# Kernel optimization log

Measured on AMD Instinct MI355X. Metric: run time of the kernel, lower is better.

## Reference

```python
import jax, jax.numpy as jnp
import numpy as np

N = 50000       # num nodes
E = 800000      # num edges
F_NODE = 128    # input node feature dim
F_EDGE = 32     # input edge feature dim
H = 64          # hidden dim (heads=1)
NEG_SLOPE = 0.2 # GAT leaky-relu slope


def _segment_softmax(scores, seg, num_segments):
    # numerically stable softmax over edges grouped by destination node
    m = jax.ops.segment_max(scores, seg, num_segments=num_segments)
    ex = jnp.exp(scores - m[seg])
    denom = jax.ops.segment_sum(ex, seg, num_segments=num_segments)
    return ex / (denom[seg] + 1e-16)


def _egat_conv(x, src, dst, eattr, W, We, a_src, a_dst, a_e, b):
    # PyG-style GAT layer with edge features (heads=1, no self loops).
    xp = x @ W                      # [N, H] projected nodes
    ep = eattr @ We                 # [E, H] projected edges (returned as new edge feats)
    score = (xp @ a_src)[src] + (xp @ a_dst)[dst] + ep @ a_e  # [E]
    score = jax.nn.leaky_relu(score, NEG_SLOPE)
    alpha = _segment_softmax(score, dst, N)                    # [E]
    out = jax.ops.segment_sum(alpha[:, None] * xp[src], dst, num_segments=N) + b
    return out, alpha, ep


def setup_inputs() -> dict:
    key = jax.random.key(0)
    ks = jax.random.split(key, 24)
    inp = {
        "x": jax.random.normal(ks[0], (N, F_NODE), jnp.float32),
        "edge_index": jax.random.randint(ks[1], (2, E), 0, N, jnp.int64),
        "edge_attr": jax.random.normal(ks[2], (E, F_EDGE), jnp.float32),
    }
    def glorot(k, shape):
        fan = shape[0] + shape[-1]
        return jax.random.normal(k, shape, jnp.float32) * jnp.sqrt(2.0 / fan)
    dims = [(F_NODE, F_EDGE), (H, H), (H, H)]
    i = 3
    for li, (din, dedge) in enumerate(dims, start=1):
        inp[f"W{li}"] = glorot(ks[i], (din, H)); i += 1
        inp[f"We{li}"] = glorot(ks[i], (dedge, H)); i += 1
        inp[f"as{li}"] = glorot(ks[i], (H,)); i += 1
        inp[f"ad{li}"] = glorot(ks[i], (H,)); i += 1
        inp[f"ae{li}"] = glorot(ks[i], (H,)); i += 1
        inp[f"b{li}"] = jnp.zeros((H,), jnp.float32)
    inp["Wc"] = glorot(ks[i], (H, 1)); i += 1
    inp["bc"] = jnp.zeros((1,), jnp.float32)
    return inp


def reference(x, edge_index, edge_attr,
              W1, We1, as1, ad1, ae1, b1,
              W2, We2, as2, ad2, ae2, b2,
              W3, We3, as3, ad3, ae3, b3,
              Wc, bc):
    src, dst = edge_index[0], edge_index[1]
    # layer 1 (edge feats projected F_EDGE -> H, reused as next edge_attr)
    x1, _, e1 = _egat_conv(x, src, dst, edge_attr, W1, We1, as1, ad1, ae1, b1)
    x1 = jax.nn.relu(x1)  # dropout is identity in eval mode
    # layer 2
    x2, _, e2 = _egat_conv(x1, src, dst, e1, W2, We2, as2, ad2, ae2, b2)
    x2 = jax.nn.relu(x2)
    # layer 3
    x3, _, _ = _egat_conv(x2, src, dst, e2, W3, We3, as3, ad3, ae3, b3)
    x3 = jax.nn.relu(x3)
    return x3 @ Wc + bc  # [N, 1]
```

## Files before the change

kernel.cpp:

```cpp
#include <hip/hip_runtime.h>
#include <hip/hip_fp16.h>
#include <math.h>

#define NN 50000
#define NE 800000
#define FN 128
#define FE 32
#define HD 64
#define NB 49
#define GP ((NN + 127) / 128)
#define EB ((NE + 511) / 512)

typedef unsigned long long u64;
typedef unsigned short u16;

__global__ void k_vecs_zero(const float* __restrict__ We1, const float* __restrict__ We2,
                            const float* __restrict__ We3, const float* __restrict__ ae1,
                            const float* __restrict__ ae2, const float* __restrict__ ae3,
                            float* __restrict__ v123, int* __restrict__ deg) {
  const int i = blockIdx.x * blockDim.x + threadIdx.x;
  if (i < NN) deg[i] = 0;
  if (blockIdx.x != 0) return;
  __shared__ float u2[HD], u3[HD], u23[HD];
  const int t = threadIdx.x;
  if (t < HD) {
    float s2 = 0.f, s3 = 0.f;
    for (int j = 0; j < HD; ++j) {
      s2 += We2[t * HD + j] * ae2[j];
      s3 += We3[t * HD + j] * ae3[j];
    }
    u2[t] = s2; u3[t] = s3;
  }
  __syncthreads();
  if (t < HD) {
    float s23 = 0.f;
    for (int j = 0; j < HD; ++j) s23 += We2[t * HD + j] * u3[j];
    u23[t] = s23;
  }
  __syncthreads();
  if (t < FE) {
    float a = 0.f, b = 0.f, c = 0.f;
    for (int j = 0; j < HD; ++j) {
      float w = We1[t * HD + j];
      a += w * ae1[j];
      b += w * u2[j];
      c += w * u23[j];
    }
    v123[t] = a; v123[32 + t] = b; v123[64 + t] = c;
  }
}

__device__ __forceinline__ u64 make_trec(const float* __restrict__ eattr,
                                         const float* __restrict__ v123,
                                         int s, int e) {
  const float4* ea = (const float4*)(eattr + (size_t)e * FE);
  float a = 0.f, b = 0.f, c = 0.f;
#pragma unroll
  for (int q = 0; q < FE / 4; ++q) {
    float4 xv = ea[q];
    const float* v1 = v123 + q * 4;
    const float* v2 = v123 + 32 + q * 4;
    const float* v3 = v123 + 64 + q * 4;
    a += xv.x * v1[0] + xv.y * v1[1] + xv.z * v1[2] + xv.w * v1[3];
    b += xv.x * v2[0] + xv.y * v2[1] + xv.z * v2[2] + xv.w * v2[3];
    c += xv.x * v3[0] + xv.y * v3[1] + xv.z * v3[2] + xv.w * v3[3];
  }
  return (u64)(u16)s
       | ((u64)__half_as_ushort(__float2half_rn(a)) << 16)
       | ((u64)__half_as_ushort(__float2half_rn(b)) << 32)
       | ((u64)__half_as_ushort(__float2half_rn(c)) << 48);
}

__global__ __launch_bounds__(256, 8) void k_edge(
    const int* __restrict__ srcA, const int* __restrict__ dstA,
    const float* __restrict__ eattr, const float* __restrict__ v123,
    int* __restrict__ deg, u16* __restrict__ rank, u64* __restrict__ trec) {
  const int t = threadIdx.x;
  const int base = blockIdx.x * 512;
  const int e0 = base + t;
  const int e1 = base + 256 + t;
  const bool ok0 = e0 < NE, ok1 = e1 < NE;

  int d0 = 0, d1 = 0, s0 = 0, s1 = 0;
  if (ok0) d0 = dstA[e0];
  if (ok1) d1 = dstA[e1];
  int r0 = 0, r1 = 0;
  if (ok0) r0 = atomicAdd(&deg[d0], 1);
  if (ok1) r1 = atomicAdd(&deg[d1], 1);
  if (ok0) s0 = srcA[e0];
  if (ok1) s1 = srcA[e1];

  if (ok0) trec[e0] = make_trec(eattr, v123, s0, e0);
  if (ok1) trec[e1] = make_trec(eattr, v123, s1, e1);

  if (ok0) rank[e0] = (u16)r0;
  if (ok1) rank[e1] = (u16)r1;
}

__global__ __launch_bounds__(256) void k_scanA(const int* __restrict__ deg,
                                               int* __restrict__ bsum) {
  __shared__ int ws[4];
  const int t = threadIdx.x, lane = t & 63, wid = t >> 6;
  const int i0 = blockIdx.x * 1024 + t * 4;
  int s = 0;
#pragma unroll
  for (int j = 0; j < 4; ++j) {
    int i = i0 + j;
    if (i < NN) s += deg[i];
  }
#pragma unroll
  for (int off = 32; off; off >>= 1) s += __shfl_xor(s, off);
  if (lane == 0) ws[wid] = s;
  __syncthreads();
  if (t == 0) bsum[blockIdx.x] = ws[0] + ws[1] + ws[2] + ws[3];
}

__global__ __launch_bounds__(256) void k_scanB(const int* __restrict__ deg,
                                               const int* __restrict__ bsum,
                                               int* __restrict__ row_ptr) {
  __shared__ int blockOff;
  __shared__ int wOff[4];
  const int b = blockIdx.x;
  const int t = threadIdx.x, lane = t & 63, wid = t >> 6;
  if (t < 64) {
    int v = (t < NB) ? bsum[t] : 0;
    int p = v;
#pragma unroll
    for (int off = 1; off < 64; off <<= 1) {
      int u = __shfl_up(p, off);
      if (lane >= off) p += u;
    }
    if (t == b) blockOff = p - v;
    if (b == 0 && t == NB - 1) row_ptr[NN] = p;
  }
  __syncthreads();
  const int i0 = b * 1024 + t * 4;
  int v[4];
#pragma unroll
  for (int j = 0; j < 4; ++j) {
    int i = i0 + j;
    v[j] = (i < NN) ? deg[i] : 0;
  }
  int s = v[0] + v[1] + v[2] + v[3];
  int p = s;
#pragma unroll
  for (int off = 1; off < 64; off <<= 1) {
    int u = __shfl_up(p, off);
    if (lane >= off) p += u;
  }
  if (lane == 63) wOff[wid] = p;
  __syncthreads();
  int woff = 0;
  for (int wq = 0; wq < wid; ++wq) woff += wOff[wq];
  int excl = blockOff + woff + (p - s);
#pragma unroll
  for (int j = 0; j < 4; ++j) {
    int i = i0 + j;
    if (i < NN) row_ptr[i] = excl;
    excl += v[j];
  }
}

__global__ __launch_bounds__(256) void k_gemm_scatter(
    const float* __restrict__ x, const float* __restrict__ W,
    const float* __restrict__ asv, const float* __restrict__ adv,
    __half* __restrict__ xph, float* __restrict__ ssrc, float* __restrict__ sdst,
    const int* __restrict__ dstA, const u16* __restrict__ rank,
    const int* __restrict__ row_ptr, const u64* __restrict__ trec,
    u64* __restrict__ aos) {
  const int t = threadIdx.x;
  if (blockIdx.x >= GP) {
    const int base = (blockIdx.x - GP) * 512;
    const int e0 = base + t;
    const int e1 = base + 256 + t;
    if (e0 < NE) aos[row_ptr[dstA[e0]] + (int)rank[e0]] = trec[e0];
    if (e1 < NE) aos[row_ptr[dstA[e1]] + (int)rank[e1]] = trec[e1];
    return;
  }
  const int w = t >> 6, l = t & 63;
  const int g = w * 4 + (l >> 4);
  const int rr = g * 8;
  const int c0 = (l & 15) * 4;
  const int row0 = blockIdx.x * 128;

  int xoff[8];
#pragma unroll
  for (int i = 0; i < 8; ++i) {
    int gr = row0 + rr + i;
    xoff[i] = (gr < NN ? gr : NN - 1) * FN;
  }

  float acc[8][4];
#pragma unroll
  for (int i = 0; i < 8; ++i)
#pragma unroll
    for (int j = 0; j < 4; ++j) acc[i][j] = 0.f;

  for (int k = 0; k < FN; k += 4) {
    float wv[4][4];
#pragma unroll
    for (int kk = 0; kk < 4; ++kk) {
      float4 wq = *(const float4*)(W + (k + kk) * HD + c0);
      wv[kk][0] = wq.x; wv[kk][1] = wq.y; wv[kk][2] = wq.z; wv[kk][3] = wq.w;
    }
#pragma unroll
    for (int i = 0; i < 8; ++i) {
      float4 a = *(const float4*)(x + xoff[i] + k);
#pragma unroll
      for (int j = 0; j < 4; ++j)
        acc[i][j] += a.x * wv[0][j] + a.y * wv[1][j] + a.z * wv[2][j] + a.w * wv[3][j];
    }
  }

  float as4[4], ad4[4];
#pragma unroll
  for (int j = 0; j < 4; ++j) { as4[j] = asv[c0 + j]; ad4[j] = adv[c0 + j]; }
#pragma unroll
  for (int i = 0; i < 8; ++i) {
    int gr = row0 + rr + i;
    float ps = 0.f, pd = 0.f;
#pragma unroll
    for (int j = 0; j < 4; ++j) {
      ps += acc[i][j] * as4[j];
      pd += acc[i][j] * ad4[j];
    }
#pragma unroll
    for (int off = 1; off < 16; off <<= 1) {
      ps += __shfl_xor(ps, off);
      pd += __shfl_xor(pd, off);
    }
    if (gr < NN) {
      union { __half2 h2[2]; float2 f2; } u;
      u.h2[0] = __floats2half2_rn(acc[i][0], acc[i][1]);
      u.h2[1] = __floats2half2_rn(acc[i][2], acc[i][3]);
      *(float2*)(xph + (size_t)gr * HD + c0) = u.f2;
      if ((l & 15) == 0) { ssrc[gr] = ps; sdst[gr] = pd; }
    }
  }
}

template <int TSEL>
__global__ __launch_bounds__(256) void k_agg_proj(
    const int* __restrict__ row_ptr, const u64* __restrict__ aos,
    const __half* __restrict__ xin, const float* __restrict__ ssrc_in,
    const float* __restrict__ sdst_in, const float* __restrict__ bias,
    const float* __restrict__ Wn, const float* __restrict__ asn,
    const float* __restrict__ adn, __half* __restrict__ xout,
    float* __restrict__ ssrc_out, float* __restrict__ sdst_out) {
  __shared__ __half swh[HD * HD];
  const int t = threadIdx.x;
  for (int i = t; i < HD * HD; i += 256) swh[i] = __float2half_rn(Wn[i]);

  const int gw = (blockIdx.x * blockDim.x + t) >> 6;
  const int lane = t & 63;
  const int g = lane >> 3;
  const int q = lane & 7;
  const int n = gw * 8 + g;
  const bool act = n < NN;
  int beg = 0, end = 0;
  float sd = 0.f;
  if (act) { beg = row_ptr[n]; end = row_ptr[n + 1]; sd = sdst_in[n]; }

  float dsum = 0.f;
  float4 o0 = make_float4(0.f, 0.f, 0.f, 0.f);
  float4 o1 = make_float4(0.f, 0.f, 0.f, 0.f);
  for (int base = beg; base < end; base += 16) {
    const int p0 = base + q, p1 = base + 8 + q;
    float pe0 = 0.f, pe1 = 0.f;
    int s0 = 0, s1 = 0;
    if (p0 < end) {
      u64 r = aos[p0];
      s0 = (int)(r & 0xFFFFu);
      float tt = __half2float(__ushort_as_half((u16)((r >> (16 * TSEL)) & 0xFFFFu)));
      float raw = ssrc_in[s0] + sd + tt;
      raw = raw > 0.f ? raw : 0.2f * raw;
      pe0 = __expf(raw);
    }
    if (p1 < end) {
      u64 r = aos[p1];
      s1 = (int)(r & 0xFFFFu);
      float tt = __half2float(__ushort_as_half((u16)((r >> (16 * TSEL)) & 0xFFFFu)));
      float raw = ssrc_in[s1] + sd + tt;
      raw = raw > 0.f ? raw : 0.2f * raw;
      pe1 = __expf(raw);
    }
    dsum += pe0 + pe1;
#pragma unroll
    for (int j = 0; j < 8; ++j) {
      const int sl = g * 8 + j;
      float pa = __shfl(pe0, sl);
      int sa = __shfl(s0, sl);
      float pb = __shfl(pe1, sl);
      int sb = __shfl(s1, sl);
      union { float4 f4; __half2 h2[4]; } ua, ub;
      ua.f4 = ((const float4*)(xin + (size_t)sa * HD))[q];
      ub.f4 = ((const float4*)(xin + (size_t)sb * HD))[q];
      float2 a0 = __half22float2(ua.h2[0]);
      float2 a1 = __half22float2(ua.h2[1]);
      float2 a2 = __half22float2(ua.h2[2]);
      float2 a3 = __half22float2(ua.h2[3]);
      o0.x += pa * a0.x; o0.y += pa * a0.y; o0.z += pa * a1.x; o0.w += pa * a1.y;
      o1.x += pa * a2.x; o1.y += pa * a2.y; o1.z += pa * a3.x; o1.w += pa * a3.y;
      float2 b0 = __half22float2(ub.h2[0]);
      float2 b1 = __half22float2(ub.h2[1]);
      float2 b2 = __half22float2(ub.h2[2]);
      float2 b3 = __half22float2(ub.h2[3]);
      o0.x += pb * b0.x; o0.y += pb * b0.y; o0.z += pb * b1.x; o0.w += pb * b1.y;
      o1.x += pb * b2.x; o1.y += pb * b2.y; o1.z += pb * b3.x; o1.w += pb * b3.y;
    }
  }
#pragma unroll
  for (int off = 1; off < 8; off <<= 1) dsum += __shfl_xor(dsum, off);

  const float inv = 1.f / (dsum + 1e-16f);
  const float4 b0 = ((const float4*)bias)[q * 2];
  const float4 b1 = ((const float4*)bias)[q * 2 + 1];
  float vreg[8];
  vreg[0] = fmaxf(o0.x * inv + b0.x, 0.f);
  vreg[1] = fmaxf(o0.y * inv + b0.y, 0.f);
  vreg[2] = fmaxf(o0.z * inv + b0.z, 0.f);
  vreg[3] = fmaxf(o0.w * inv + b0.w, 0.f);
  vreg[4] = fmaxf(o1.x * inv + b1.x, 0.f);
  vreg[5] = fmaxf(o1.y * inv + b1.y, 0.f);
  vreg[6] = fmaxf(o1.z * inv + b1.z, 0.f);
  vreg[7] = fmaxf(o1.w * inv + b1.w, 0.f);

  __syncthreads();

  float out8[8] = {0.f, 0.f, 0.f, 0.f, 0.f, 0.f, 0.f, 0.f};
#pragma unroll
  for (int kq = 0; kq < 8; ++kq) {
#pragma unroll
    for (int m = 0; m < 8; ++m) {
      float vb = __shfl(vreg[m], (lane & 56) | kq);
      union { float4 f4; __half2 h2[4]; } uw;
      uw.f4 = *(const float4*)(swh + (kq * 8 + m) * HD + q * 8);
      float2 w0 = __half22float2(uw.h2[0]);
      float2 w1 = __half22float2(uw.h2[1]);
      float2 w2 = __half22float2(uw.h2[2]);
      float2 w3 = __half22float2(uw.h2[3]);
      out8[0] += vb * w0.x; out8[1] += vb * w0.y;
      out8[2] += vb * w1.x; out8[3] += vb * w1.y;
      out8[4] += vb * w2.x; out8[5] += vb * w2.y;
      out8[6] += vb * w3.x; out8[7] += vb * w3.y;
    }
  }

  float ps = 0.f, pd = 0.f;
#pragma unroll
  for (int j = 0; j < 8; ++j) {
    ps += out8[j] * asn[q * 8 + j];
    pd += out8[j] * adn[q * 8 + j];
  }
#pragma unroll
  for (int off = 1; off < 8; off <<= 1) {
    ps += __shfl_xor(ps, off);
    pd += __shfl_xor(pd, off);
  }

  if (!act) return;
  union { float4 f4; __half2 h2[4]; } wv;
  wv.h2[0] = __floats2half2_rn(out8[0], out8[1]);
  wv.h2[1] = __floats2half2_rn(out8[2], out8[3]);
  wv.h2[2] = __floats2half2_rn(out8[4], out8[5]);
  wv.h2[3] = __floats2half2_rn(out8[6], out8[7]);
  ((float4*)(xout + (size_t)n * HD))[q] = wv.f4;
  if (q == 0) { ssrc_out[n] = ps; sdst_out[n] = pd; }
}

template <int TSEL>
__global__ __launch_bounds__(256) void k_agg_head(
    const int* __restrict__ row_ptr, const u64* __restrict__ aos,
    const __half* __restrict__ xin, const float* __restrict__ ssrc_in,
    const float* __restrict__ sdst_in, const float* __restrict__ bias,
    const float* __restrict__ Wc, const float* __restrict__ bc,
    float* __restrict__ outf) {
  const int gw = (blockIdx.x * blockDim.x + threadIdx.x) >> 6;
  const int lane = threadIdx.x & 63;
  const int g = lane >> 3;
  const int q = lane & 7;
  const int n = gw * 8 + g;
  const bool act = n < NN;
  int beg = 0, end = 0;
  float sd = 0.f;
  if (act) { beg = row_ptr[n]; end = row_ptr[n + 1]; sd = sdst_in[n]; }

  float dsum = 0.f;
  float4 o0 = make_float4(0.f, 0.f, 0.f, 0.f);
  float4 o1 = make_float4(0.f, 0.f, 0.f, 0.f);
  for (int base = beg; base < end; base += 16) {
    const int p0 = base + q, p1 = base + 8 + q;
    float pe0 = 0.f, pe1 = 0.f;
    int s0 = 0, s1 = 0;
    if (p0 < end) {
      u64 r = aos[p0];
      s0 = (int)(r & 0xFFFFu);
      float tt = __half2float(__ushort_as_half((u16)((r >> (16 * TSEL)) & 0xFFFFu)));
      float raw = ssrc_in[s0] + sd + tt;
      raw = raw > 0.f ? raw : 0.2f * raw;
      pe0 = __expf(raw);
    }
    if (p1 < end) {
      u64 r = aos[p1];
      s1 = (int)(r & 0xFFFFu);
      float tt = __half2float(__ushort_as_half((u16)((r >> (16 * TSEL)) & 0xFFFFu)));
      float raw = ssrc_in[s1] + sd + tt;
      raw = raw > 0.f ? raw : 0.2f * raw;
      pe1 = __expf(raw);
    }
    dsum += pe0 + pe1;
#pragma unroll
    for (int j = 0; j < 8; ++j) {
      const int sl = g * 8 + j;
      float pa = __shfl(pe0, sl);
      int sa = __shfl(s0, sl);
      float pb = __shfl(pe1, sl);
      int sb = __shfl(s1, sl);
      union { float4 f4; __half2 h2[4]; } ua, ub;
      ua.f4 = ((const float4*)(xin + (size_t)sa * HD))[q];
      ub.f4 = ((const float4*)(xin + (size_t)sb * HD))[q];
      float2 a0 = __half22float2(ua.h2[0]);
      float2 a1 = __half22float2(ua.h2[1]);
      float2 a2 = __half22float2(ua.h2[2]);
      float2 a3 = __half22float2(ua.h2[3]);
      o0.x += pa * a0.x; o0.y += pa * a0.y; o0.z += pa * a1.x; o0.w += pa * a1.y;
      o1.x += pa * a2.x; o1.y += pa * a2.y; o1.z += pa * a3.x; o1.w += pa * a3.y;
      float2 b0 = __half22float2(ub.h2[0]);
      float2 b1 = __half22float2(ub.h2[1]);
      float2 b2 = __half22float2(ub.h2[2]);
      float2 b3 = __half22float2(ub.h2[3]);
      o0.x += pb * b0.x; o0.y += pb * b0.y; o0.z += pb * b1.x; o0.w += pb * b1.y;
      o1.x += pb * b2.x; o1.y += pb * b2.y; o1.z += pb * b3.x; o1.w += pb * b3.y;
    }
  }
#pragma unroll
  for (int off = 1; off < 8; off <<= 1) dsum += __shfl_xor(dsum, off);

  if (!act) return;
  const float inv = 1.f / (dsum + 1e-16f);
  const float4 b0 = ((const float4*)bias)[q * 2];
  const float4 b1 = ((const float4*)bias)[q * 2 + 1];
  const float4 w0 = ((const float4*)Wc)[q * 2];
  const float4 w1 = ((const float4*)Wc)[q * 2 + 1];
  float c = fmaxf(o0.x * inv + b0.x, 0.f) * w0.x +
            fmaxf(o0.y * inv + b0.y, 0.f) * w0.y +
            fmaxf(o0.z * inv + b0.z, 0.f) * w0.z +
            fmaxf(o0.w * inv + b0.w, 0.f) * w0.w +
            fmaxf(o1.x * inv + b1.x, 0.f) * w1.x +
            fmaxf(o1.y * inv + b1.y, 0.f) * w1.y +
            fmaxf(o1.z * inv + b1.z, 0.f) * w1.z +
            fmaxf(o1.w * inv + b1.w, 0.f) * w1.w;
#pragma unroll
  for (int off = 1; off < 8; off <<= 1) c += __shfl_xor(c, off);
  if (q == 0) outf[n] = c + bc[0];
}

extern "C" void kernel_launch(void* const* d_in, const int* in_sizes, int n_in,
                              void* d_out, int out_size, void* d_ws, size_t ws_size,
                              hipStream_t stream) {
  const float* x     = (const float*)d_in[0];
  const int*   ei    = (const int*)d_in[1];
  const float* eattr = (const float*)d_in[2];
  const float* W1  = (const float*)d_in[3];
  const float* We1 = (const float*)d_in[4];
  const float* as1 = (const float*)d_in[5];
  const float* ad1 = (const float*)d_in[6];
  const float* ae1 = (const float*)d_in[7];
  const float* b1  = (const float*)d_in[8];
  const float* W2  = (const float*)d_in[9];
  const float* We2 = (const float*)d_in[10];
  const float* as2 = (const float*)d_in[11];
  const float* ad2 = (const float*)d_in[12];
  const float* ae2 = (const float*)d_in[13];
  const float* b2  = (const float*)d_in[14];
  const float* W3  = (const float*)d_in[15];
  const float* We3 = (const float*)d_in[16];
  const float* as3 = (const float*)d_in[17];
  const float* ad3 = (const float*)d_in[18];
  const float* ae3 = (const float*)d_in[19];
  const float* b3  = (const float*)d_in[20];
  const float* Wc  = (const float*)d_in[21];
  const float* bc  = (const float*)d_in[22];

  const int* srcA = ei;
  const int* dstA = ei + NE;
  float* outf = (float*)d_out;

  char* w = (char*)d_ws;
  auto alloc = [&](size_t bytes) {
    char* p = w;
    w += (bytes + 255) & ~(size_t)255;
    return p;
  };
  float* v123 = (float*)alloc(96 * 4);
  u64* aos = (u64*)alloc((size_t)NE * 8);
  u64* trec = (u64*)alloc((size_t)NE * 8);
  u16* rank = (u16*)alloc((size_t)NE * 2);
  int* row_ptr = (int*)alloc((size_t)(NN + 1) * 4);
  int* deg = (int*)alloc((size_t)NN * 4);
  int* bsum = (int*)alloc((size_t)NB * 4);
  __half* xpA = (__half*)alloc((size_t)NN * HD * 2);
  __half* xpB = (__half*)alloc((size_t)NN * HD * 2);
  float* ssrcA = (float*)alloc((size_t)NN * 4);
  float* sdstA = (float*)alloc((size_t)NN * 4);
  float* ssrcB = (float*)alloc((size_t)NN * 4);
  float* sdstB = (float*)alloc((size_t)NN * 4);

  const int gN = (NN + 255) / 256;
  const int gA = ((NN + 7) / 8 * 64 + 255) / 256;

  k_vecs_zero<<<gN, 256, 0, stream>>>(We1, We2, We3, ae1, ae2, ae3, v123, deg);
  k_edge<<<EB, 256, 0, stream>>>(srcA, dstA, eattr, v123, deg, rank, trec);
  k_scanA<<<NB, 256, 0, stream>>>(deg, bsum);
  k_scanB<<<NB, 256, 0, stream>>>(deg, bsum, row_ptr);
  k_gemm_scatter<<<GP + EB, 256, 0, stream>>>(x, W1, as1, ad1, xpA, ssrcA, sdstA,
                                              dstA, rank, row_ptr, trec, aos);
  k_agg_proj<1><<<gA, 256, 0, stream>>>(row_ptr, aos, xpA, ssrcA, sdstA, b1,
                                        W2, as2, ad2, xpB, ssrcB, sdstB);
  k_agg_proj<2><<<gA, 256, 0, stream>>>(row_ptr, aos, xpB, ssrcB, sdstB, b2,
                                        W3, as3, ad3, xpA, ssrcA, sdstA);
  k_agg_head<3><<<gA, 256, 0, stream>>>(row_ptr, aos, xpA, ssrcA, sdstA, b3,
                                        Wc, bc, outf);
}
```

Baseline: 176.1 us.

## Privatize degree counters into sixteen slices and fuse layer-1 GEMM with edge pass

Degree counting now uses sixteen private copies of the counter array, one per group of edge blocks, so atomic contention on hot destination nodes is spread out. The scan kernels sum the slices and turn each slice into a per-slice base offset used by a new standalone scatter kernel. The layer-1 node GEMM moves from the scatter kernel into the edge/atomic kernel, so it runs in the same launch as the edge pass. In exchange the zeroing and scans touch sixteen times more counter memory, and the scan writes per-slice offsets with strided accesses.

```diff
diff --git a/kernel.cpp b/kernel.cpp
--- a/kernel.cpp
+++ b/kernel.cpp
@@ -7,6 +7,7 @@
 #define FN 128
 #define FE 32
 #define HD 64
+#define NS 16
 #define NB 49
 #define GP ((NN + 127) / 128)
 #define EB ((NE + 511) / 512)
@@ -19,7 +20,7 @@
                             const float* __restrict__ ae2, const float* __restrict__ ae3,
                             float* __restrict__ v123, int* __restrict__ deg) {
   const int i = blockIdx.x * blockDim.x + threadIdx.x;
-  if (i < NN) deg[i] = 0;
+  if (i < NS * NN) deg[i] = 0;
   if (blockIdx.x != 0) return;
   __shared__ float u2[HD], u3[HD], u23[HD];
   const int t = threadIdx.x;
@@ -71,30 +72,98 @@
        | ((u64)__half_as_ushort(__float2half_rn(c)) << 48);
 }
 
-__global__ __launch_bounds__(256, 8) void k_edge(
+__global__ __launch_bounds__(256) void k_mega2(
+    const float* __restrict__ x, const float* __restrict__ W,
+    const float* __restrict__ asv, const float* __restrict__ adv,
+    __half* __restrict__ xph, float* __restrict__ ssrc, float* __restrict__ sdst,
     const int* __restrict__ srcA, const int* __restrict__ dstA,
     const float* __restrict__ eattr, const float* __restrict__ v123,
     int* __restrict__ deg, u16* __restrict__ rank, u64* __restrict__ trec) {
   const int t = threadIdx.x;
-  const int base = blockIdx.x * 512;
-  const int e0 = base + t;
-  const int e1 = base + 256 + t;
-  const bool ok0 = e0 < NE, ok1 = e1 < NE;
-
-  int d0 = 0, d1 = 0, s0 = 0, s1 = 0;
-  if (ok0) d0 = dstA[e0];
-  if (ok1) d1 = dstA[e1];
-  int r0 = 0, r1 = 0;
-  if (ok0) r0 = atomicAdd(&deg[d0], 1);
-  if (ok1) r1 = atomicAdd(&deg[d1], 1);
-  if (ok0) s0 = srcA[e0];
-  if (ok1) s1 = srcA[e1];
-
-  if (ok0) trec[e0] = make_trec(eattr, v123, s0, e0);
-  if (ok1) trec[e1] = make_trec(eattr, v123, s1, e1);
-
-  if (ok0) rank[e0] = (u16)r0;
-  if (ok1) rank[e1] = (u16)r1;
+  if (blockIdx.x >= GP) {
+    const int k = blockIdx.x - GP;
+    const int base = k * 512;
+    const int psh = (k & (NS - 1)) * NN;
+    const int e0 = base + t;
+    const int e1 = base + 256 + t;
+    const bool ok0 = e0 < NE, ok1 = e1 < NE;
+
+    int d0 = 0, d1 = 0, s0 = 0, s1 = 0;
+    if (ok0) d0 = dstA[e0];
+    if (ok1) d1 = dstA[e1];
+    int r0 = 0, r1 = 0;
+    if (ok0) r0 = atomicAdd(&deg[psh + d0], 1);
+    if (ok1) r1 = atomicAdd(&deg[psh + d1], 1);
+    if (ok0) s0 = srcA[e0];
+    if (ok1) s1 = srcA[e1];
+
+    if (ok0) trec[e0] = make_trec(eattr, v123, s0, e0);
+    if (ok1) trec[e1] = make_trec(eattr, v123, s1, e1);
+
+    if (ok0) rank[e0] = (u16)r0;
+    if (ok1) rank[e1] = (u16)r1;
+    return;
+  }
+  const int w = t >> 6, l = t & 63;
+  const int g = w * 4 + (l >> 4);
+  const int rr = g * 8;
+  const int c0 = (l & 15) * 4;
+  const int row0 = blockIdx.x * 128;
+
+  int xoff[8];
+#pragma unroll
+  for (int i = 0; i < 8; ++i) {
+    int gr = row0 + rr + i;
+    xoff[i] = (gr < NN ? gr : NN - 1) * FN;
+  }
+
+  float acc[8][4];
+#pragma unroll
+  for (int i = 0; i < 8; ++i)
+#pragma unroll
+    for (int j = 0; j < 4; ++j) acc[i][j] = 0.f;
+
+  for (int k = 0; k < FN; k += 4) {
+    float wv[4][4];
+#pragma unroll
+    for (int kk = 0; kk < 4; ++kk) {
+      float4 wq = *(const float4*)(W + (k + kk) * HD + c0);
+      wv[kk][0] = wq.x; wv[kk][1] = wq.y; wv[kk][2] = wq.z; wv[kk][3] = wq.w;
+    }
+#pragma unroll
+    for (int i = 0; i < 8; ++i) {
+      float4 a = *(const float4*)(x + xoff[i] + k);
+#pragma unroll
+      for (int j = 0; j < 4; ++j)
+        acc[i][j] += a.x * wv[0][j] + a.y * wv[1][j] + a.z * wv[2][j] + a.w * wv[3][j];
+    }
+  }
+
+  float as4[4], ad4[4];
+#pragma unroll
+  for (int j = 0; j < 4; ++j) { as4[j] = asv[c0 + j]; ad4[j] = adv[c0 + j]; }
+#pragma unroll
+  for (int i = 0; i < 8; ++i) {
+    int gr = row0 + rr + i;
+    float ps = 0.f, pd = 0.f;
+#pragma unroll
+    for (int j = 0; j < 4; ++j) {
+      ps += acc[i][j] * as4[j];
+      pd += acc[i][j] * ad4[j];
+    }
+#pragma unroll
+    for (int off = 1; off < 16; off <<= 1) {
+      ps += __shfl_xor(ps, off);
+      pd += __shfl_xor(pd, off);
+    }
+    if (gr < NN) {
+      union { __half2 h2[2]; float2 f2; } u;
+      u.h2[0] = __floats2half2_rn(acc[i][0], acc[i][1]);
+      u.h2[1] = __floats2half2_rn(acc[i][2], acc[i][3]);
+      *(float2*)(xph + (size_t)gr * HD + c0) = u.f2;
+      if ((l & 15) == 0) { ssrc[gr] = ps; sdst[gr] = pd; }
+    }
+  }
 }
 
 __global__ __launch_bounds__(256) void k_scanA(const int* __restrict__ deg,
@@ -103,10 +172,12 @@
   const int t = threadIdx.x, lane = t & 63, wid = t >> 6;
   const int i0 = blockIdx.x * 1024 + t * 4;
   int s = 0;
-#pragma unroll
-  for (int j = 0; j < 4; ++j) {
-    int i = i0 + j;
-    if (i < NN) s += deg[i];
+  if (i0 < NN) {
+#pragma unroll
+    for (int p = 0; p < NS; ++p) {
+      int4 v = *(const int4*)(deg + p * NN + i0);
+      s += v.x + v.y + v.z + v.w;
+    }
   }
 #pragma unroll
   for (int off = 32; off; off >>= 1) s += __shfl_xor(s, off);
@@ -115,7 +186,7 @@
   if (t == 0) bsum[blockIdx.x] = ws[0] + ws[1] + ws[2] + ws[3];
 }
 
-__global__ __launch_bounds__(256) void k_scanB(const int* __restrict__ deg,
+__global__ __launch_bounds__(256) void k_scanB(int* __restrict__ deg,
                                                const int* __restrict__ bsum,
                                                int* __restrict__ row_ptr) {
   __shared__ int blockOff;
@@ -136,10 +207,16 @@
   __syncthreads();
   const int i0 = b * 1024 + t * 4;
   int v[4];
-#pragma unroll
-  for (int j = 0; j < 4; ++j) {
-    int i = i0 + j;
-    v[j] = (i < NN) ? deg[i] : 0;
+  if (i0 < NN) {
+    int4 acc = make_int4(0, 0, 0, 0);
+#pragma unroll
+    for (int p = 0; p < NS; ++p) {
+      int4 dv = *(const int4*)(deg + p * NN + i0);
+      acc.x += dv.x; acc.y += dv.y; acc.z += dv.z; acc.w += dv.w;
+    }
+    v[0] = acc.x; v[1] = acc.y; v[2] = acc.z; v[3] = acc.w;
+  } else {
+    v[0] = v[1] = v[2] = v[3] = 0;
   }
   int s = v[0] + v[1] + v[2] + v[3];
   int p = s;
@@ -156,87 +233,31 @@
 #pragma unroll
   for (int j = 0; j < 4; ++j) {
     int i = i0 + j;
-    if (i < NN) row_ptr[i] = excl;
-    excl += v[j];
-  }
-}
-
-__global__ __launch_bounds__(256) void k_gemm_scatter(
-    const float* __restrict__ x, const float* __restrict__ W,
-    const float* __restrict__ asv, const float* __restrict__ adv,
-    __half* __restrict__ xph, float* __restrict__ ssrc, float* __restrict__ sdst,
-    const int* __restrict__ dstA, const u16* __restrict__ rank,
-    const int* __restrict__ row_ptr, const u64* __restrict__ trec,
-    u64* __restrict__ aos) {
+    if (i < NN) {
+      row_ptr[i] = excl;
+      int run = excl;
+#pragma unroll
+      for (int ps = 0; ps < NS; ++ps) {
+        int dv = deg[ps * NN + i];
+        deg[ps * NN + i] = run;
+        run += dv;
+      }
+      excl += v[j];
+    }
+  }
+}
+
+__global__ void k_scatter(const int* __restrict__ dstA, const u16* __restrict__ rank,
+                          const int* __restrict__ sbase, const u64* __restrict__ trec,
+                          u64* __restrict__ aos) {
+  const int k = blockIdx.x;
+  const int base = k * 512;
+  const int psh = (k & (NS - 1)) * NN;
   const int t = threadIdx.x;
-  if (blockIdx.x >= GP) {
-    const int base = (blockIdx.x - GP) * 512;
-    const int e0 = base + t;
-    const int e1 = base + 256 + t;
-    if (e0 < NE) aos[row_ptr[dstA[e0]] + (int)rank[e0]] = trec[e0];
-    if (e1 < NE) aos[row_ptr[dstA[e1]] + (int)rank[e1]] = trec[e1];
-    return;
-  }
-  const int w = t >> 6, l = t & 63;
-  const int g = w * 4 + (l >> 4);
-  const int rr = g * 8;
-  const int c0 = (l & 15) * 4;
-  const int row0 = blockIdx.x * 128;
-
-  int xoff[8];
-#pragma unroll
-  for (int i = 0; i < 8; ++i) {
-    int gr = row0 + rr + i;
-    xoff[i] = (gr < NN ? gr : NN - 1) * FN;
-  }
-
-  float acc[8][4];
-#pragma unroll
-  for (int i = 0; i < 8; ++i)
-#pragma unroll
-    for (int j = 0; j < 4; ++j) acc[i][j] = 0.f;
-
-  for (int k = 0; k < FN; k += 4) {
-    float wv[4][4];
-#pragma unroll
-    for (int kk = 0; kk < 4; ++kk) {
-      float4 wq = *(const float4*)(W + (k + kk) * HD + c0);
-      wv[kk][0] = wq.x; wv[kk][1] = wq.y; wv[kk][2] = wq.z; wv[kk][3] = wq.w;
-    }
-#pragma unroll
-    for (int i = 0; i < 8; ++i) {
-      float4 a = *(const float4*)(x + xoff[i] + k);
-#pragma unroll
-      for (int j = 0; j < 4; ++j)
-        acc[i][j] += a.x * wv[0][j] + a.y * wv[1][j] + a.z * wv[2][j] + a.w * wv[3][j];
-    }
-  }
-
-  float as4[4], ad4[4];
-#pragma unroll
-  for (int j = 0; j < 4; ++j) { as4[j] = asv[c0 + j]; ad4[j] = adv[c0 + j]; }
-#pragma unroll
-  for (int i = 0; i < 8; ++i) {
-    int gr = row0 + rr + i;
-    float ps = 0.f, pd = 0.f;
-#pragma unroll
-    for (int j = 0; j < 4; ++j) {
-      ps += acc[i][j] * as4[j];
-      pd += acc[i][j] * ad4[j];
-    }
-#pragma unroll
-    for (int off = 1; off < 16; off <<= 1) {
-      ps += __shfl_xor(ps, off);
-      pd += __shfl_xor(pd, off);
-    }
-    if (gr < NN) {
-      union { __half2 h2[2]; float2 f2; } u;
-      u.h2[0] = __floats2half2_rn(acc[i][0], acc[i][1]);
-      u.h2[1] = __floats2half2_rn(acc[i][2], acc[i][3]);
-      *(float2*)(xph + (size_t)gr * HD + c0) = u.f2;
-      if ((l & 15) == 0) { ssrc[gr] = ps; sdst[gr] = pd; }
-    }
-  }
+  const int e0 = base + t;
+  const int e1 = base + 256 + t;
+  if (e0 < NE) aos[sbase[psh + dstA[e0]] + (int)rank[e0]] = trec[e0];
+  if (e1 < NE) aos[sbase[psh + dstA[e1]] + (int)rank[e1]] = trec[e1];
 }
 
 template <int TSEL>
@@ -497,7 +518,7 @@
   u64* trec = (u64*)alloc((size_t)NE * 8);
   u16* rank = (u16*)alloc((size_t)NE * 2);
   int* row_ptr = (int*)alloc((size_t)(NN + 1) * 4);
-  int* deg = (int*)alloc((size_t)NN * 4);
+  int* deg = (int*)alloc((size_t)NS * NN * 4);
   int* bsum = (int*)alloc((size_t)NB * 4);
   __half* xpA = (__half*)alloc((size_t)NN * HD * 2);
   __half* xpB = (__half*)alloc((size_t)NN * HD * 2);
@@ -506,15 +527,15 @@
   float* ssrcB = (float*)alloc((size_t)NN * 4);
   float* sdstB = (float*)alloc((size_t)NN * 4);
 
-  const int gN = (NN + 255) / 256;
+  const int gZ = (NS * NN + 255) / 256;
   const int gA = ((NN + 7) / 8 * 64 + 255) / 256;
 
-  k_vecs_zero<<<gN, 256, 0, stream>>>(We1, We2, We3, ae1, ae2, ae3, v123, deg);
-  k_edge<<<EB, 256, 0, stream>>>(srcA, dstA, eattr, v123, deg, rank, trec);
+  k_vecs_zero<<<gZ, 256, 0, stream>>>(We1, We2, We3, ae1, ae2, ae3, v123, deg);
+  k_mega2<<<GP + EB, 256, 0, stream>>>(x, W1, as1, ad1, xpA, ssrcA, sdstA,
+                                       srcA, dstA, eattr, v123, deg, rank, trec);
   k_scanA<<<NB, 256, 0, stream>>>(deg, bsum);
   k_scanB<<<NB, 256, 0, stream>>>(deg, bsum, row_ptr);
-  k_gemm_scatter<<<GP + EB, 256, 0, stream>>>(x, W1, as1, ad1, xpA, ssrcA, sdstA,
-                                              dstA, rank, row_ptr, trec, aos);
+  k_scatter<<<EB, 256, 0, stream>>>(dstA, rank, deg, trec, aos);
   k_agg_proj<1><<<gA, 256, 0, stream>>>(row_ptr, aos, xpA, ssrcA, sdstA, b1,
                                         W2, as2, ad2, xpB, ssrcB, sdstB);
   k_agg_proj<2><<<gA, 256, 0, stream>>>(row_ptr, aos, xpB, ssrcB, sdstB, b2,
```

Result: faster. 172.3 us (-2.1%).

## Replace global-atomic CSR build with two-pass bucketed radix partition by destination

Applied to the files above, without the earlier changes.

The CSR construction no longer does per-edge global atomics on a degree array. It now builds per-block shared-memory histograms over 196 coarse destination buckets of 256 nodes each, scans them, and scatters edge records into the buckets with shared atomics. A final per-bucket kernel does a local counting sort into the CSR array and writes row_ptr. This is meant to cut contended global atomics and the random scatter. In exchange it adds an extra pass over an intermediate 8-byte record buffer and produces a different within-row edge order.

```diff
diff --git a/kernel.cpp b/kernel.cpp
--- a/kernel.cpp
+++ b/kernel.cpp
@@ -7,48 +7,17 @@
 #define FN 128
 #define FE 32
 #define HD 64
-#define NB 49
+#define NBKT 196
+#define EPB 2048
+#define NSB ((NE + EPB - 1) / EPB)
+#define EPT (EPB / 256)
+#define CNT_N (NBKT * NSB)
+#define SCB 2048
+#define NB2 ((CNT_N + SCB - 1) / SCB)
 #define GP ((NN + 127) / 128)
-#define EB ((NE + 511) / 512)
 
 typedef unsigned long long u64;
 typedef unsigned short u16;
-
-__global__ void k_vecs_zero(const float* __restrict__ We1, const float* __restrict__ We2,
-                            const float* __restrict__ We3, const float* __restrict__ ae1,
-                            const float* __restrict__ ae2, const float* __restrict__ ae3,
-                            float* __restrict__ v123, int* __restrict__ deg) {
-  const int i = blockIdx.x * blockDim.x + threadIdx.x;
-  if (i < NN) deg[i] = 0;
-  if (blockIdx.x != 0) return;
-  __shared__ float u2[HD], u3[HD], u23[HD];
-  const int t = threadIdx.x;
-  if (t < HD) {
-    float s2 = 0.f, s3 = 0.f;
-    for (int j = 0; j < HD; ++j) {
-      s2 += We2[t * HD + j] * ae2[j];
-      s3 += We3[t * HD + j] * ae3[j];
-    }
-    u2[t] = s2; u3[t] = s3;
-  }
-  __syncthreads();
-  if (t < HD) {
-    float s23 = 0.f;
-    for (int j = 0; j < HD; ++j) s23 += We2[t * HD + j] * u3[j];
-    u23[t] = s23;
-  }
-  __syncthreads();
-  if (t < FE) {
-    float a = 0.f, b = 0.f, c = 0.f;
-    for (int j = 0; j < HD; ++j) {
-      float w = We1[t * HD + j];
-      a += w * ae1[j];
-      b += w * u2[j];
-      c += w * u23[j];
-    }
-    v123[t] = a; v123[32 + t] = b; v123[64 + t] = c;
-  }
-}
 
 __device__ __forceinline__ u64 make_trec(const float* __restrict__ eattr,
                                          const float* __restrict__ v123,
@@ -71,42 +40,65 @@
        | ((u64)__half_as_ushort(__float2half_rn(c)) << 48);
 }
 
-__global__ __launch_bounds__(256, 8) void k_edge(
-    const int* __restrict__ srcA, const int* __restrict__ dstA,
-    const float* __restrict__ eattr, const float* __restrict__ v123,
-    int* __restrict__ deg, u16* __restrict__ rank, u64* __restrict__ trec) {
+__global__ __launch_bounds__(256) void k_count(
+    const int* __restrict__ dstA, int* __restrict__ cnt,
+    const float* __restrict__ We1, const float* __restrict__ We2,
+    const float* __restrict__ We3, const float* __restrict__ ae1,
+    const float* __restrict__ ae2, const float* __restrict__ ae3,
+    float* __restrict__ v123) {
+  __shared__ int hist[NBKT];
   const int t = threadIdx.x;
-  const int base = blockIdx.x * 512;
-  const int e0 = base + t;
-  const int e1 = base + 256 + t;
-  const bool ok0 = e0 < NE, ok1 = e1 < NE;
-
-  int d0 = 0, d1 = 0, s0 = 0, s1 = 0;
-  if (ok0) d0 = dstA[e0];
-  if (ok1) d1 = dstA[e1];
-  int r0 = 0, r1 = 0;
-  if (ok0) r0 = atomicAdd(&deg[d0], 1);
-  if (ok1) r1 = atomicAdd(&deg[d1], 1);
-  if (ok0) s0 = srcA[e0];
-  if (ok1) s1 = srcA[e1];
-
-  if (ok0) trec[e0] = make_trec(eattr, v123, s0, e0);
-  if (ok1) trec[e1] = make_trec(eattr, v123, s1, e1);
-
-  if (ok0) rank[e0] = (u16)r0;
-  if (ok1) rank[e1] = (u16)r1;
-}
-
-__global__ __launch_bounds__(256) void k_scanA(const int* __restrict__ deg,
-                                               int* __restrict__ bsum) {
+  const int blk = blockIdx.x;
+  if (t < NBKT) hist[t] = 0;
+  __syncthreads();
+  const int base = blk * EPB;
+#pragma unroll 1
+  for (int it = 0; it < EPT; ++it) {
+    int e = base + it * 256 + t;
+    if (e < NE) atomicAdd(&hist[dstA[e] >> 8], 1);
+  }
+  __syncthreads();
+  if (t < NBKT) cnt[t * NSB + blk] = hist[t];
+
+  if (blk != 0) return;
+  __shared__ float u2[HD], u3[HD], u23[HD];
+  if (t < HD) {
+    float s2 = 0.f, s3 = 0.f;
+    for (int j = 0; j < HD; ++j) {
+      s2 += We2[t * HD + j] * ae2[j];
+      s3 += We3[t * HD + j] * ae3[j];
+    }
+    u2[t] = s2; u3[t] = s3;
+  }
+  __syncthreads();
+  if (t < HD) {
+    float s23 = 0.f;
+    for (int j = 0; j < HD; ++j) s23 += We2[t * HD + j] * u3[j];
+    u23[t] = s23;
+  }
+  __syncthreads();
+  if (t < FE) {
+    float a = 0.f, b = 0.f, c = 0.f;
+    for (int j = 0; j < HD; ++j) {
+      float w = We1[t * HD + j];
+      a += w * ae1[j];
+      b += w * u2[j];
+      c += w * u23[j];
+    }
+    v123[t] = a; v123[32 + t] = b; v123[64 + t] = c;
+  }
+}
+
+__global__ __launch_bounds__(256) void k_scanA2(const int* __restrict__ cnt,
+                                                int* __restrict__ bsum) {
   __shared__ int ws[4];
   const int t = threadIdx.x, lane = t & 63, wid = t >> 6;
-  const int i0 = blockIdx.x * 1024 + t * 4;
+  const int i0 = blockIdx.x * SCB + t * 8;
   int s = 0;
 #pragma unroll
-  for (int j = 0; j < 4; ++j) {
+  for (int j = 0; j < 8; ++j) {
     int i = i0 + j;
-    if (i < NN) s += deg[i];
+    if (i < CNT_N) s += cnt[i];
   }
 #pragma unroll
   for (int off = 32; off; off >>= 1) s += __shfl_xor(s, off);
@@ -115,15 +107,14 @@
   if (t == 0) bsum[blockIdx.x] = ws[0] + ws[1] + ws[2] + ws[3];
 }
 
-__global__ __launch_bounds__(256) void k_scanB(const int* __restrict__ deg,
-                                               const int* __restrict__ bsum,
-                                               int* __restrict__ row_ptr) {
+__global__ __launch_bounds__(256) void k_scanB2(int* __restrict__ cnt,
+                                                const int* __restrict__ bsum) {
   __shared__ int blockOff;
   __shared__ int wOff[4];
   const int b = blockIdx.x;
   const int t = threadIdx.x, lane = t & 63, wid = t >> 6;
   if (t < 64) {
-    int v = (t < NB) ? bsum[t] : 0;
+    int v = (t < NB2) ? bsum[t] : 0;
     int p = v;
 #pragma unroll
     for (int off = 1; off < 64; off <<= 1) {
@@ -131,17 +122,18 @@
       if (lane >= off) p += u;
     }
     if (t == b) blockOff = p - v;
-    if (b == 0 && t == NB - 1) row_ptr[NN] = p;
-  }
-  __syncthreads();
-  const int i0 = b * 1024 + t * 4;
-  int v[4];
-#pragma unroll
-  for (int j = 0; j < 4; ++j) {
+  }
+  __syncthreads();
+  const int i0 = b * SCB + t * 8;
+  int v[8];
+#pragma unroll
+  for (int j = 0; j < 8; ++j) {
     int i = i0 + j;
-    v[j] = (i < NN) ? deg[i] : 0;
-  }
-  int s = v[0] + v[1] + v[2] + v[3];
+    v[j] = (i < CNT_N) ? cnt[i] : 0;
+  }
+  int s = 0;
+#pragma unroll
+  for (int j = 0; j < 8; ++j) s += v[j];
   int p = s;
 #pragma unroll
   for (int off = 1; off < 64; off <<= 1) {
@@ -154,34 +146,47 @@
   for (int wq = 0; wq < wid; ++wq) woff += wOff[wq];
   int excl = blockOff + woff + (p - s);
 #pragma unroll
-  for (int j = 0; j < 4; ++j) {
+  for (int j = 0; j < 8; ++j) {
     int i = i0 + j;
-    if (i < NN) row_ptr[i] = excl;
-    excl += v[j];
-  }
-}
-
-__global__ __launch_bounds__(256) void k_gemm_scatter(
+    if (i < CNT_N) { cnt[i] = excl; excl += v[j]; }
+  }
+}
+
+__global__ __launch_bounds__(256) void k_mega3(
     const float* __restrict__ x, const float* __restrict__ W,
     const float* __restrict__ asv, const float* __restrict__ adv,
     __half* __restrict__ xph, float* __restrict__ ssrc, float* __restrict__ sdst,
-    const int* __restrict__ dstA, const u16* __restrict__ rank,
-    const int* __restrict__ row_ptr, const u64* __restrict__ trec,
-    u64* __restrict__ aos) {
+    const int* __restrict__ srcA, const int* __restrict__ dstA,
+    const float* __restrict__ eattr, const float* __restrict__ v123,
+    const int* __restrict__ gbase, u64* __restrict__ btrec,
+    u16* __restrict__ bdst) {
+  __shared__ int off[NBKT];
   const int t = threadIdx.x;
-  if (blockIdx.x >= GP) {
-    const int base = (blockIdx.x - GP) * 512;
-    const int e0 = base + t;
-    const int e1 = base + 256 + t;
-    if (e0 < NE) aos[row_ptr[dstA[e0]] + (int)rank[e0]] = trec[e0];
-    if (e1 < NE) aos[row_ptr[dstA[e1]] + (int)rank[e1]] = trec[e1];
+  if (blockIdx.x < NSB) {
+    const int blk = blockIdx.x;
+    if (t < NBKT) off[t] = gbase[t * NSB + blk];
+    __syncthreads();
+    const int base = blk * EPB;
+#pragma unroll 1
+    for (int it = 0; it < EPT; ++it) {
+      int e = base + it * 256 + t;
+      if (e < NE) {
+        int d = dstA[e];
+        int s = srcA[e];
+        u64 r = make_trec(eattr, v123, s, e);
+        int pos = atomicAdd(&off[d >> 8], 1);
+        btrec[pos] = r;
+        bdst[pos] = (u16)(d & 255);
+      }
+    }
     return;
   }
+  const int pb = blockIdx.x - NSB;
   const int w = t >> 6, l = t & 63;
   const int g = w * 4 + (l >> 4);
   const int rr = g * 8;
   const int c0 = (l & 15) * 4;
-  const int row0 = blockIdx.x * 128;
+  const int row0 = pb * 128;
 
   int xoff[8];
 #pragma unroll
@@ -225,9 +230,9 @@
       pd += acc[i][j] * ad4[j];
     }
 #pragma unroll
-    for (int off = 1; off < 16; off <<= 1) {
-      ps += __shfl_xor(ps, off);
-      pd += __shfl_xor(pd, off);
+    for (int off2 = 1; off2 < 16; off2 <<= 1) {
+      ps += __shfl_xor(ps, off2);
+      pd += __shfl_xor(pd, off2);
     }
     if (gr < NN) {
       union { __half2 h2[2]; float2 f2; } u;
@@ -236,6 +241,45 @@
       *(float2*)(xph + (size_t)gr * HD + c0) = u.f2;
       if ((l & 15) == 0) { ssrc[gr] = ps; sdst[gr] = pd; }
     }
+  }
+}
+
+__global__ __launch_bounds__(256) void k_bucket(
+    const int* __restrict__ gbase, const u64* __restrict__ btrec,
+    const u16* __restrict__ bdst, int* __restrict__ row_ptr,
+    u64* __restrict__ aos) {
+  __shared__ int hist[256], off2[256];
+  __shared__ int wsum[4];
+  const int b = blockIdx.x;
+  const int t = threadIdx.x, lane = t & 63, wid = t >> 6;
+  const int s = gbase[b * NSB];
+  const int e = (b + 1 < NBKT) ? gbase[(b + 1) * NSB] : NE;
+  hist[t] = 0;
+  __syncthreads();
+  for (int p = s + t; p < e; p += 256) atomicAdd(&hist[(int)bdst[p]], 1);
+  __syncthreads();
+  int v = hist[t];
+  int pfx = v;
+#pragma unroll
+  for (int o = 1; o < 64; o <<= 1) {
+    int u = __shfl_up(pfx, o);
+    if (lane >= o) pfx += u;
+  }
+  if (lane == 63) wsum[wid] = pfx;
+  __syncthreads();
+  int woff = 0;
+  for (int wq = 0; wq < wid; ++wq) woff += wsum[wq];
+  const int excl = woff + pfx - v;
+  off2[t] = excl;
+  const int n = b * 256 + t;
+  if (n < NN) row_ptr[n] = s + excl;
+  if (b == 0 && t == 0) row_ptr[NN] = NE;
+  __syncthreads();
+  for (int p = s + t; p < e; p += 256) {
+    u64 r = btrec[p];
+    int d8 = (int)bdst[p];
+    int pos = s + atomicAdd(&off2[d8], 1);
+    aos[pos] = r;
   }
 }
 
@@ -494,11 +538,11 @@
   };
   float* v123 = (float*)alloc(96 * 4);
   u64* aos = (u64*)alloc((size_t)NE * 8);
-  u64* trec = (u64*)alloc((size_t)NE * 8);
-  u16* rank = (u16*)alloc((size_t)NE * 2);
+  u64* btrec = (u64*)alloc((size_t)NE * 8);
+  u16* bdst = (u16*)alloc((size_t)NE * 2);
   int* row_ptr = (int*)alloc((size_t)(NN + 1) * 4);
-  int* deg = (int*)alloc((size_t)NN * 4);
-  int* bsum = (int*)alloc((size_t)NB * 4);
+  int* cnt = (int*)alloc((size_t)CNT_N * 4);
+  int* bsum = (int*)alloc((size_t)NB2 * 4);
   __half* xpA = (__half*)alloc((size_t)NN * HD * 2);
   __half* xpB = (__half*)alloc((size_t)NN * HD * 2);
   float* ssrcA = (float*)alloc((size_t)NN * 4);
@@ -506,15 +550,14 @@
   float* ssrcB = (float*)alloc((size_t)NN * 4);
   float* sdstB = (float*)alloc((size_t)NN * 4);
 
-  const int gN = (NN + 255) / 256;
   const int gA = ((NN + 7) / 8 * 64 + 255) / 256;
 
-  k_vecs_zero<<<gN, 256, 0, stream>>>(We1, We2, We3, ae1, ae2, ae3, v123, deg);
-  k_edge<<<EB, 256, 0, stream>>>(srcA, dstA, eattr, v123, deg, rank, trec);
-  k_scanA<<<NB, 256, 0, stream>>>(deg, bsum);
-  k_scanB<<<NB, 256, 0, stream>>>(deg, bsum, row_ptr);
-  k_gemm_scatter<<<GP + EB, 256, 0, stream>>>(x, W1, as1, ad1, xpA, ssrcA, sdstA,
-                                              dstA, rank, row_ptr, trec, aos);
+  k_count<<<NSB, 256, 0, stream>>>(dstA, cnt, We1, We2, We3, ae1, ae2, ae3, v123);
+  k_scanA2<<<NB2, 256, 0, stream>>>(cnt, bsum);
+  k_scanB2<<<NB2, 256, 0, stream>>>(cnt, bsum);
+  k_mega3<<<NSB + GP, 256, 0, stream>>>(x, W1, as1, ad1, xpA, ssrcA, sdstA,
+                                        srcA, dstA, eattr, v123, cnt, btrec, bdst);
+  k_bucket<<<NBKT, 256, 0, stream>>>(cnt, btrec, bdst, row_ptr, aos);
   k_agg_proj<1><<<gA, 256, 0, stream>>>(row_ptr, aos, xpA, ssrcA, sdstA, b1,
                                         W2, as2, ad2, xpB, ssrcB, sdstB);
   k_agg_proj<2><<<gA, 256, 0, stream>>>(row_ptr, aos, xpB, ssrcB, sdstB, b2,
```

New measurement: 171.3 us. 2.8% less time.

## Fuse layer-1 GEMM with edge pass; coalesce edge-attr loads via cooperative reduction

Applied to the files above, without the earlier changes.

Moves the layer-1 node projection GEMM into the same launch as the per-edge degree counting and score-term computation, and makes the CSR scatter its own kernel after the scan. The edge pass now has 8 lanes read one edge's 32 attributes cooperatively in contiguous float4 chunks and reduces with shuffles, replacing strided per-thread row reads. This is meant to overlap the compute-bound GEMM with the memory- and atomic-bound edge work and to coalesce edge_attr reads. In exchange it adds shuffle work, and the scatter stays a separate launch. NT=NE/64 assumes NE is divisible by 64, which holds here.

```diff
diff --git a/kernel.cpp b/kernel.cpp
--- a/kernel.cpp
+++ b/kernel.cpp
@@ -9,7 +9,9 @@
 #define HD 64
 #define NB 49
 #define GP ((NN + 127) / 128)
-#define EB ((NE + 511) / 512)
+#define NT (NE / 64)
+#define EB2 ((NT + 7) / 8)
+#define GE ((NE + 255) / 256)
 
 typedef unsigned long long u64;
 typedef unsigned short u16;
@@ -50,51 +52,116 @@
   }
 }
 
-__device__ __forceinline__ u64 make_trec(const float* __restrict__ eattr,
-                                         const float* __restrict__ v123,
-                                         int s, int e) {
-  const float4* ea = (const float4*)(eattr + (size_t)e * FE);
-  float a = 0.f, b = 0.f, c = 0.f;
-#pragma unroll
-  for (int q = 0; q < FE / 4; ++q) {
-    float4 xv = ea[q];
-    const float* v1 = v123 + q * 4;
-    const float* v2 = v123 + 32 + q * 4;
-    const float* v3 = v123 + 64 + q * 4;
-    a += xv.x * v1[0] + xv.y * v1[1] + xv.z * v1[2] + xv.w * v1[3];
-    b += xv.x * v2[0] + xv.y * v2[1] + xv.z * v2[2] + xv.w * v2[3];
-    c += xv.x * v3[0] + xv.y * v3[1] + xv.z * v3[2] + xv.w * v3[3];
-  }
-  return (u64)(u16)s
-       | ((u64)__half_as_ushort(__float2half_rn(a)) << 16)
-       | ((u64)__half_as_ushort(__float2half_rn(b)) << 32)
-       | ((u64)__half_as_ushort(__float2half_rn(c)) << 48);
-}
-
-__global__ __launch_bounds__(256, 8) void k_edge(
+__global__ __launch_bounds__(256) void k_mega4(
+    const float* __restrict__ x, const float* __restrict__ W,
+    const float* __restrict__ asv, const float* __restrict__ adv,
+    __half* __restrict__ xph, float* __restrict__ ssrc, float* __restrict__ sdst,
     const int* __restrict__ srcA, const int* __restrict__ dstA,
     const float* __restrict__ eattr, const float* __restrict__ v123,
     int* __restrict__ deg, u16* __restrict__ rank, u64* __restrict__ trec) {
   const int t = threadIdx.x;
-  const int base = blockIdx.x * 512;
-  const int e0 = base + t;
-  const int e1 = base + 256 + t;
-  const bool ok0 = e0 < NE, ok1 = e1 < NE;
-
-  int d0 = 0, d1 = 0, s0 = 0, s1 = 0;
-  if (ok0) d0 = dstA[e0];
-  if (ok1) d1 = dstA[e1];
-  int r0 = 0, r1 = 0;
-  if (ok0) r0 = atomicAdd(&deg[d0], 1);
-  if (ok1) r1 = atomicAdd(&deg[d1], 1);
-  if (ok0) s0 = srcA[e0];
-  if (ok1) s1 = srcA[e1];
-
-  if (ok0) trec[e0] = make_trec(eattr, v123, s0, e0);
-  if (ok1) trec[e1] = make_trec(eattr, v123, s1, e1);
-
-  if (ok0) rank[e0] = (u16)r0;
-  if (ok1) rank[e1] = (u16)r1;
+  if (blockIdx.x >= GP) {
+    const int kb = blockIdx.x - GP;
+    const int w = t >> 6, lane = t & 63;
+    const int g = lane >> 3, q = lane & 7;
+    const float4 v1q = *(const float4*)(v123 + q * 4);
+    const float4 v2q = *(const float4*)(v123 + 32 + q * 4);
+    const float4 v3q = *(const float4*)(v123 + 64 + q * 4);
+    const int perm = 8 * q + g;
+#pragma unroll
+    for (int it = 0; it < 2; ++it) {
+      const int tIdx = kb * 8 + w * 2 + it;
+      if (tIdx < NT) {
+        const int E0 = tIdx * 64;
+        const int e = E0 + perm;
+        const int d = dstA[e];
+        const int s = srcA[e];
+        const int r = atomicAdd(&deg[d], 1);
+        float ra = 0.f, rb = 0.f, rc = 0.f;
+#pragma unroll
+        for (int k = 0; k < 8; ++k) {
+          const float4 xv =
+              *(const float4*)(eattr + (size_t)(E0 + 8 * k + g) * FE + q * 4);
+          float a = xv.x * v1q.x + xv.y * v1q.y + xv.z * v1q.z + xv.w * v1q.w;
+          float b = xv.x * v2q.x + xv.y * v2q.y + xv.z * v2q.z + xv.w * v2q.w;
+          float c = xv.x * v3q.x + xv.y * v3q.y + xv.z * v3q.z + xv.w * v3q.w;
+#pragma unroll
+          for (int off = 1; off < 8; off <<= 1) {
+            a += __shfl_xor(a, off);
+            b += __shfl_xor(b, off);
+            c += __shfl_xor(c, off);
+          }
+          if (q == k) { ra = a; rb = b; rc = c; }
+        }
+        trec[e] = (u64)(u16)s
+                | ((u64)__half_as_ushort(__float2half_rn(ra)) << 16)
+                | ((u64)__half_as_ushort(__float2half_rn(rb)) << 32)
+                | ((u64)__half_as_ushort(__float2half_rn(rc)) << 48);
+        rank[e] = (u16)r;
+      }
+    }
+    return;
+  }
+  const int w = t >> 6, l = t & 63;
+  const int g = w * 4 + (l >> 4);
+  const int rr = g * 8;
+  const int c0 = (l & 15) * 4;
+  const int row0 = blockIdx.x * 128;
+
+  int xoff[8];
+#pragma unroll
+  for (int i = 0; i < 8; ++i) {
+    int gr = row0 + rr + i;
+    xoff[i] = (gr < NN ? gr : NN - 1) * FN;
+  }
+
+  float acc[8][4];
+#pragma unroll
+  for (int i = 0; i < 8; ++i)
+#pragma unroll
+    for (int j = 0; j < 4; ++j) acc[i][j] = 0.f;
+
+  for (int k = 0; k < FN; k += 4) {
+    float wv[4][4];
+#pragma unroll
+    for (int kk = 0; kk < 4; ++kk) {
+      float4 wq = *(const float4*)(W + (k + kk) * HD + c0);
+      wv[kk][0] = wq.x; wv[kk][1] = wq.y; wv[kk][2] = wq.z; wv[kk][3] = wq.w;
+    }
+#pragma unroll
+    for (int i = 0; i < 8; ++i) {
+      float4 a = *(const float4*)(x + xoff[i] + k);
+#pragma unroll
+      for (int j = 0; j < 4; ++j)
+        acc[i][j] += a.x * wv[0][j] + a.y * wv[1][j] + a.z * wv[2][j] + a.w * wv[3][j];
+    }
+  }
+
+  float as4[4], ad4[4];
+#pragma unroll
+  for (int j = 0; j < 4; ++j) { as4[j] = asv[c0 + j]; ad4[j] = adv[c0 + j]; }
+#pragma unroll
+  for (int i = 0; i < 8; ++i) {
+    int gr = row0 + rr + i;
+    float ps = 0.f, pd = 0.f;
+#pragma unroll
+    for (int j = 0; j < 4; ++j) {
+      ps += acc[i][j] * as4[j];
+      pd += acc[i][j] * ad4[j];
+    }
+#pragma unroll
+    for (int off = 1; off < 16; off <<= 1) {
+      ps += __shfl_xor(ps, off);
+      pd += __shfl_xor(pd, off);
+    }
+    if (gr < NN) {
+      union { __half2 h2[2]; float2 f2; } u;
+      u.h2[0] = __floats2half2_rn(acc[i][0], acc[i][1]);
+      u.h2[1] = __floats2half2_rn(acc[i][2], acc[i][3]);
+      *(float2*)(xph + (size_t)gr * HD + c0) = u.f2;
+      if ((l & 15) == 0) { ssrc[gr] = ps; sdst[gr] = pd; }
+    }
+  }
 }
 
 __global__ __launch_bounds__(256) void k_scanA(const int* __restrict__ deg,
@@ -161,82 +228,12 @@
   }
 }
 
-__global__ __launch_bounds__(256) void k_gemm_scatter(
-    const float* __restrict__ x, const float* __restrict__ W,
-    const float* __restrict__ asv, const float* __restrict__ adv,
-    __half* __restrict__ xph, float* __restrict__ ssrc, float* __restrict__ sdst,
-    const int* __restrict__ dstA, const u16* __restrict__ rank,
-    const int* __restrict__ row_ptr, const u64* __restrict__ trec,
-    u64* __restrict__ aos) {
-  const int t = threadIdx.x;
-  if (blockIdx.x >= GP) {
-    const int base = (blockIdx.x - GP) * 512;
-    const int e0 = base + t;
-    const int e1 = base + 256 + t;
-    if (e0 < NE) aos[row_ptr[dstA[e0]] + (int)rank[e0]] = trec[e0];
-    if (e1 < NE) aos[row_ptr[dstA[e1]] + (int)rank[e1]] = trec[e1];
-    return;
-  }
-  const int w = t >> 6, l = t & 63;
-  const int g = w * 4 + (l >> 4);
-  const int rr = g * 8;
-  const int c0 = (l & 15) * 4;
-  const int row0 = blockIdx.x * 128;
-
-  int xoff[8];
-#pragma unroll
-  for (int i = 0; i < 8; ++i) {
-    int gr = row0 + rr + i;
-    xoff[i] = (gr < NN ? gr : NN - 1) * FN;
-  }
-
-  float acc[8][4];
-#pragma unroll
-  for (int i = 0; i < 8; ++i)
-#pragma unroll
-    for (int j = 0; j < 4; ++j) acc[i][j] = 0.f;
-
-  for (int k = 0; k < FN; k += 4) {
-    float wv[4][4];
-#pragma unroll
-    for (int kk = 0; kk < 4; ++kk) {
-      float4 wq = *(const float4*)(W + (k + kk) * HD + c0);
-      wv[kk][0] = wq.x; wv[kk][1] = wq.y; wv[kk][2] = wq.z; wv[kk][3] = wq.w;
-    }
-#pragma unroll
-    for (int i = 0; i < 8; ++i) {
-      float4 a = *(const float4*)(x + xoff[i] + k);
-#pragma unroll
-      for (int j = 0; j < 4; ++j)
-        acc[i][j] += a.x * wv[0][j] + a.y * wv[1][j] + a.z * wv[2][j] + a.w * wv[3][j];
-    }
-  }
-
-  float as4[4], ad4[4];
-#pragma unroll
-  for (int j = 0; j < 4; ++j) { as4[j] = asv[c0 + j]; ad4[j] = adv[c0 + j]; }
-#pragma unroll
-  for (int i = 0; i < 8; ++i) {
-    int gr = row0 + rr + i;
-    float ps = 0.f, pd = 0.f;
-#pragma unroll
-    for (int j = 0; j < 4; ++j) {
-      ps += acc[i][j] * as4[j];
-      pd += acc[i][j] * ad4[j];
-    }
-#pragma unroll
-    for (int off = 1; off < 16; off <<= 1) {
-      ps += __shfl_xor(ps, off);
-      pd += __shfl_xor(pd, off);
-    }
-    if (gr < NN) {
-      union { __half2 h2[2]; float2 f2; } u;
-      u.h2[0] = __floats2half2_rn(acc[i][0], acc[i][1]);
-      u.h2[1] = __floats2half2_rn(acc[i][2], acc[i][3]);
-      *(float2*)(xph + (size_t)gr * HD + c0) = u.f2;
-      if ((l & 15) == 0) { ssrc[gr] = ps; sdst[gr] = pd; }
-    }
-  }
+__global__ void k_scatter(const int* __restrict__ dstA, const u16* __restrict__ rank,
+                          const int* __restrict__ row_ptr, const u64* __restrict__ trec,
+                          u64* __restrict__ aos) {
+  const int e = blockIdx.x * blockDim.x + threadIdx.x;
+  if (e >= NE) return;
+  aos[row_ptr[dstA[e]] + (int)rank[e]] = trec[e];
 }
 
 template <int TSEL>
@@ -510,11 +507,11 @@
   const int gA = ((NN + 7) / 8 * 64 + 255) / 256;
 
   k_vecs_zero<<<gN, 256, 0, stream>>>(We1, We2, We3, ae1, ae2, ae3, v123, deg);
-  k_edge<<<EB, 256, 0, stream>>>(srcA, dstA, eattr, v123, deg, rank, trec);
+  k_mega4<<<GP + EB2, 256, 0, stream>>>(x, W1, as1, ad1, xpA, ssrcA, sdstA,
+                                        srcA, dstA, eattr, v123, deg, rank, trec);
   k_scanA<<<NB, 256, 0, stream>>>(deg, bsum);
   k_scanB<<<NB, 256, 0, stream>>>(deg, bsum, row_ptr);
-  k_gemm_scatter<<<GP + EB, 256, 0, stream>>>(x, W1, as1, ad1, xpA, ssrcA, sdstA,
-                                              dstA, rank, row_ptr, trec, aos);
+  k_scatter<<<GE, 256, 0, stream>>>(dstA, rank, row_ptr, trec, aos);
   k_agg_proj<1><<<gA, 256, 0, stream>>>(row_ptr, aos, xpA, ssrcA, sdstA, b1,
                                         W2, as2, ad2, xpB, ssrcB, sdstB);
   k_agg_proj<2><<<gA, 256, 0, stream>>>(row_ptr, aos, xpB, ssrcB, sdstB, b2,
```

Result: faster. 151.8 us (-13.8%).
